# Performance work log

Hardware: AMD Instinct MI355X
Metric: run time of the kernel (lower is better)

Reference implementation:

```python
import jax, jax.numpy as jnp
import numpy as np

B, S, DIM, NH = 256, 64, 1024, 8
DH = DIM // NH
EPS = 1e-6
LN_EPS = 1e-5


def _make_hops(n):
    hops = np.zeros((n, n), dtype=np.int64)
    cur = 1
    for i in range(n):
        for j in range(i + 1, n):
            hops[i, j] = cur
            hops[j, i] = cur
            cur += 1
    return hops, cur


def setup_inputs() -> dict:
    key = jax.random.key(0)
    ks = jax.random.split(key, 8)
    hops_np, curnum = _make_hops(S)
    return {
        "q": jax.random.normal(ks[0], (B, S, DIM), dtype=jnp.float32),
        "k": jax.random.normal(ks[1], (B, S, DIM), dtype=jnp.float32),
        "v": jax.random.normal(ks[2], (B, S, DIM), dtype=jnp.float32),
        "igate_w": jax.random.normal(ks[3], (NH, 3 * DIM), dtype=jnp.float32) * 0.02,
        "igate_b": jax.random.normal(ks[4], (NH,), dtype=jnp.float32) * 0.1,
        "fgate_w": jax.random.normal(ks[5], (NH, 3 * DIM), dtype=jnp.float32) * 0.02,
        "fgate_b": jnp.linspace(3.0, 6.0, NH, dtype=jnp.float32),
        "rpe": jax.random.normal(ks[6], (curnum, DIM), dtype=jnp.float32) * 0.02,
        "ln_w": jax.random.normal(ks[7], (DIM,), dtype=jnp.float32) * 0.1,
        "ln_b": jnp.zeros((DIM,), dtype=jnp.float32),
        "hops": jnp.asarray(hops_np),
    }


def _mlstm_forward(q, k, v, igate_w, igate_b, fgate_w, fgate_b, rpe, ln_w, ln_b, hops):
    Bq, Sq, _ = q.shape
    pos_emb = rpe[hops]                                   # (S, S, DIM)
    gate_in = jnp.concatenate([q, k, v], axis=-1)         # (B, S, 3*DIM)
    ig = gate_in @ igate_w.T + igate_b                    # (B, S, NH)
    fg = gate_in @ fgate_w.T + fgate_b                    # (B, S, NH)
    ig = jnp.transpose(ig, (0, 2, 1))                     # (B, NH, S)
    fg = jnp.transpose(fg, (0, 2, 1))                     # (B, NH, S)

    qh = q.reshape(Bq, Sq, NH, DH).transpose(0, 2, 1, 3)  # (B, NH, S, DH)
    kh = k.reshape(Bq, Sq, NH, DH).transpose(0, 2, 1, 3)
    vh = v.reshape(Bq, Sq, NH, DH).transpose(0, 2, 1, 3)

    # log forget gates, cumulative sum with a leading zero
    log_f = jax.nn.log_sigmoid(fg)                        # (B, NH, S)
    csum = jnp.cumsum(log_f, axis=-1)
    csum = jnp.concatenate([jnp.zeros((Bq, NH, 1), csum.dtype), csum], axis=-1)  # (B,NH,S+1)
    lfm = csum[:, :, :, None] - csum[:, :, None, :]       # (B, NH, S+1, S+1)
    ltr = jnp.tril(jnp.ones((Sq, Sq), dtype=bool))
    log_fg_matrix = jnp.where(ltr, lfm[:, :, 1:, 1:], -jnp.inf)  # (B, NH, S, S)

    log_D = log_fg_matrix + ig[:, :, None, :]             # add i-gate per column
    max_log_D = jnp.max(log_D, axis=-1, keepdims=True)    # rowwise stabilization
    D = jnp.exp(log_D - max_log_D)                        # (B, NH, S, S)

    k_scaled = kh / np.sqrt(DH).astype(np.float32)
    pe = pos_emb.reshape(Sq, Sq, NH, DH)
    k_hop = jnp.einsum('bhvc,vmhc->bhvm', qh, pe)         # (B, NH, S, S)
    qk = jnp.einsum('bhsd,bhtd->bhst', qh, k_scaled)      # (B, NH, S, S)
    C = (qk + k_hop) * D

    normalizer = jnp.maximum(jnp.abs(jnp.sum(C, axis=-1, keepdims=True)), jnp.exp(-max_log_D))
    Cn = C / (normalizer + EPS)
    h = Cn @ vh                                           # (B, NH, S, DH)

    # MultiHeadLayerNorm == group_norm with NH groups: normalize each head over DH
    mu = jnp.mean(h, axis=-1, keepdims=True)
    var = jnp.mean(jnp.square(h - mu), axis=-1, keepdims=True)
    hn = (h - mu) / jnp.sqrt(var + LN_EPS)
    w = (1.0 + ln_w).reshape(NH, DH)                      # residual weight: 1 + w
    b = ln_b.reshape(NH, DH)
    hn = hn * w[None, :, None, :] + b[None, :, None, :]
    return hn.transpose(0, 2, 1, 3).reshape(Bq, Sq, DIM)


def reference(q, k, v, igate_w, igate_b, fgate_w, fgate_b, rpe, ln_w, ln_b, hops):
    return _mlstm_forward(q, k, v, igate_w, igate_b, fgate_w, fgate_b, rpe, ln_w, ln_b, hops)
```

## Files before the change

kernel.cpp:

```cpp
#include <hip/hip_runtime.h>
#include <math.h>

#define BB 256
#define SS 64
#define DIMM 1024
#define NHH 8
#define DHH 128

typedef short bf16x8 __attribute__((ext_vector_type(8)));
typedef float f32x4 __attribute__((ext_vector_type(4)));

__device__ __forceinline__ unsigned cvtpk(float lo, float hi) {
    unsigned r;
    asm("v_cvt_pk_bf16_f32 %0, %1, %2" : "=v"(r) : "v"(lo), "v"(hi));
    return r;
}
__device__ __forceinline__ unsigned pk2(float lo, float hi) { return cvtpk(lo, hi); }
__device__ __forceinline__ unsigned short f2bh(float x) {
    return (unsigned short)(cvtpk(x, 0.0f) & 0xFFFFu);
}
__device__ __forceinline__ float bf2f(unsigned short b) {
    union { unsigned u; float f; } x{((unsigned)b) << 16};
    return x.f;
}
__device__ __forceinline__ void split2(float a, float b, unsigned& hi, unsigned& lo) {
    hi = cvtpk(a, b);
    const float ha = __uint_as_float(hi << 16);
    const float hb = __uint_as_float(hi & 0xFFFF0000u);
    lo = cvtpk(a - ha, b - hb);
}
__device__ __forceinline__ float logsigf(float x) {
    return fminf(x, 0.0f) - log1pf(__expf(-fabsf(x)));
}

__global__ __launch_bounds__(256) void k_gate_mfma(
    const float* __restrict__ q, const float* __restrict__ k, const float* __restrict__ v,
    const float* __restrict__ igw, const float* __restrict__ fgw,
    float* __restrict__ part)
{
    __shared__ unsigned short Xs[64 * 264];
    __shared__ unsigned short Ws[16 * 264];
    const int b = blockIdx.x & 255;
    const int ksl = blockIdx.x >> 8;
    const int t = threadIdx.x;
    const int w = t >> 6, l = t & 63, c = l & 15, g = l >> 4;

    f32x4 acc;
    acc[0] = 0.f; acc[1] = 0.f; acc[2] = 0.f; acc[3] = 0.f;

    for (int step = 0; step < 3; ++step) {
        const int kc = ksl * 3 + step;
        const int tensor = kc >> 2;
        const float* src = (tensor == 0) ? q : (tensor == 1) ? k : v;
        src += ((size_t)b * 64) * 1024 + (kc & 3) * 256;
        {
            const int row = t >> 2, seg = t & 3;
            const float* rp = src + row * 1024;
            #pragma unroll
            for (int e = 0; e < 16; ++e) {
                const int col = e * 16 + seg * 4;
                const float4 x = *reinterpret_cast<const float4*>(rp + col);
                unsigned* dp = reinterpret_cast<unsigned*>(&Xs[row * 264 + col]);
                dp[0] = pk2(x.x, x.y); dp[1] = pk2(x.z, x.w);
            }
        }
        {
            const int o = t >> 4, wseg = t & 15;
            const int p0 = ksl * 768 + step * 256;
            const float* wp = (o < 8 ? igw + o * 3072 : fgw + (o - 8) * 3072) + p0;
            #pragma unroll
            for (int e = 0; e < 4; ++e) {
                const int col = e * 64 + wseg * 4;
                const float4 x = *reinterpret_cast<const float4*>(wp + col);
                unsigned* dp = reinterpret_cast<unsigned*>(&Ws[o * 264 + col]);
                dp[0] = pk2(x.x, x.y); dp[1] = pk2(x.z, x.w);
            }
        }
        __syncthreads();
        #pragma unroll
        for (int kk = 0; kk < 8; ++kk) {
            bf16x8 a  = *reinterpret_cast<const bf16x8*>(&Xs[(16 * w + c) * 264 + 32 * kk + 8 * g]);
            bf16x8 bw = *reinterpret_cast<const bf16x8*>(&Ws[c * 264 + 32 * kk + 8 * g]);
            acc = __builtin_amdgcn_mfma_f32_16x16x32_bf16(a, bw, acc, 0, 0, 0);
        }
        __syncthreads();
    }
    float* pb = part + (((size_t)ksl * 256 + b) * 64) * 16;
    #pragma unroll
    for (int reg = 0; reg < 4; ++reg) {
        const int s = 16 * w + 4 * g + reg;
        pb[s * 16 + c] = acc[reg];
    }
}

__global__ __launch_bounds__(256) void k_gates_final(
    const float* __restrict__ part, const float* __restrict__ igb, const float* __restrict__ fgb,
    float* __restrict__ ig_ws, float* __restrict__ csum_ws, float* __restrict__ pmax_ws)
{
    const int b = blockIdx.x;
    const int t = threadIdx.x;
    __shared__ float red[64][18];
    {
        const int s = t >> 2, oq = t & 3;
        float4 sum = make_float4(0.f, 0.f, 0.f, 0.f);
        #pragma unroll
        for (int ksl = 0; ksl < 4; ++ksl) {
            const float4 p = *reinterpret_cast<const float4*>(
                part + (((size_t)ksl * 256 + b) * 64 + s) * 16 + oq * 4);
            sum.x += p.x; sum.y += p.y; sum.z += p.z; sum.w += p.w;
        }
        red[s][oq * 4 + 0] = sum.x; red[s][oq * 4 + 1] = sum.y;
        red[s][oq * 4 + 2] = sum.z; red[s][oq * 4 + 3] = sum.w;
    }
    __syncthreads();
    if (t < 64) {
        const int s = t;
        #pragma unroll
        for (int h = 0; h < 8; ++h) {
            float ig = red[s][h]     + igb[h];
            float fg = red[s][8 + h] + fgb[h];
            float lf = logsigf(fg);
            float cs = lf;
            #pragma unroll
            for (int d = 1; d < 64; d <<= 1) {
                float o = __shfl_up(cs, (unsigned)d, 64);
                if (s >= d) cs += o;
            }
            float pm = ig - cs;
            #pragma unroll
            for (int d = 1; d < 64; d <<= 1) {
                float o = __shfl_up(pm, (unsigned)d, 64);
                if (s >= d) pm = fmaxf(pm, o);
            }
            const int base = b * NHH + h;
            ig_ws[base * SS + s] = ig;
            csum_ws[base * 65 + s + 1] = cs;
            if (s == 0) csum_ws[base * 65] = 0.0f;
            pmax_ws[base * SS + s] = pm;
        }
    }
}

__global__ __launch_bounds__(256) void k_khop(
    const float* __restrict__ q, const float* __restrict__ rpe, const int* __restrict__ hops,
    float* __restrict__ khop_ws)
{
    __shared__ unsigned short Phi[64 * 136];
    __shared__ unsigned short Plo[64 * 136];
    const int v = blockIdx.x;
    const int h = blockIdx.y;
    const int t = threadIdx.x;
    const int w = t >> 6, l = t & 63, c = l & 15, g = l >> 4;

    const int npair = (v + 1) * 64;
    unsigned* PhiU = reinterpret_cast<unsigned*>(Phi);
    unsigned* PloU = reinterpret_cast<unsigned*>(Plo);
    for (int idx = t; idx < npair; idx += 256) {
        const int m = idx >> 6, cp = idx & 63;
        const float2 x = *reinterpret_cast<const float2*>(
            rpe + (size_t)hops[v * SS + m] * DIMM + h * DHH + 2 * cp);
        unsigned hi, lo;
        split2(x.x, x.y, hi, lo);
        PhiU[m * 68 + cp] = hi;
        PloU[m * 68 + cp] = lo;
    }
    __syncthreads();

    const int ntiles = (v >> 4) + 1;
    union bfu { unsigned u[4]; bf16x8 vv; };
    #pragma unroll
    for (int ms = 0; ms < 4; ++ms) {
        const int brow = 64 * w + 16 * ms + c;
        const float* qbase = q + ((size_t)brow * SS + v) * DIMM + h * DHH + 8 * g;
        bfu qhi[4], qlo[4];
        #pragma unroll
        for (int kk = 0; kk < 4; ++kk) {
            const float4 f0 = *reinterpret_cast<const float4*>(qbase + 32 * kk);
            const float4 f1 = *reinterpret_cast<const float4*>(qbase + 32 * kk + 4);
            split2(f0.x, f0.y, qhi[kk].u[0], qlo[kk].u[0]);
            split2(f0.z, f0.w, qhi[kk].u[1], qlo[kk].u[1]);
            split2(f1.x, f1.y, qhi[kk].u[2], qlo[kk].u[2]);
            split2(f1.z, f1.w, qhi[kk].u[3], qlo[kk].u[3]);
        }
        for (int n = 0; n < ntiles; ++n) {
            f32x4 acc;
            acc[0] = 0.f; acc[1] = 0.f; acc[2] = 0.f; acc[3] = 0.f;
            #pragma unroll
            for (int kk = 0; kk < 4; ++kk) {
                const int off = (16 * n + c) * 136 + 32 * kk + 8 * g;
                bf16x8 bhi = *reinterpret_cast<const bf16x8*>(&Phi[off]);
                bf16x8 blo = *reinterpret_cast<const bf16x8*>(&Plo[off]);
                acc = __builtin_amdgcn_mfma_f32_16x16x32_bf16(qhi[kk].vv, bhi, acc, 0, 0, 0);
                acc = __builtin_amdgcn_mfma_f32_16x16x32_bf16(qlo[kk].vv, bhi, acc, 0, 0, 0);
                acc = __builtin_amdgcn_mfma_f32_16x16x32_bf16(qhi[kk].vv, blo, acc, 0, 0, 0);
            }
            #pragma unroll
            for (int reg = 0; reg < 4; ++reg) {
                const int bo = 64 * w + 16 * ms + 4 * g + reg;
                khop_ws[(((size_t)bo * NHH + h) * SS + v) * SS + 16 * n + c] = acc[reg];
            }
        }
    }
}

__global__ __launch_bounds__(256) void k_attn(
    const float* __restrict__ q, const float* __restrict__ k, const float* __restrict__ v,
    const float* __restrict__ lnw, const float* __restrict__ lnb,
    const float* __restrict__ ig_ws, const float* __restrict__ csum_ws,
    const float* __restrict__ pmax_ws, const float* __restrict__ khop_ws,
    float* __restrict__ out)
{
    __shared__ __attribute__((aligned(16))) unsigned short Kspl[2 * 64 * 136];
    __shared__ float csum_s[65];
    __shared__ float ig_s[64];
    __shared__ float pmax_s[64];
    __shared__ float lnw_s[128];
    __shared__ float lnb_s[128];

    const int bid = blockIdx.x;
    const int b = bid >> 3, h = bid & 7;
    const int t = threadIdx.x;
    const int w = t >> 6, l = t & 63, c = l & 15, g = l >> 4;
    const float rs_dh = 0.08838834764831845f;

    unsigned short* Khi = Kspl;
    unsigned short* Klo = Kspl + 64 * 136;

    float4 vreg[2][4];
    #pragma unroll
    for (int it = 0; it < 2; ++it) {
        const int u = t + 256 * it;
        const int jp = u >> 4, seg8 = u & 15;
        const float* r0 = v + ((size_t)(b * 64 + 2 * jp)) * 1024 + h * 128 + seg8 * 8;
        vreg[it][0] = *reinterpret_cast<const float4*>(r0);
        vreg[it][1] = *reinterpret_cast<const float4*>(r0 + 4);
        vreg[it][2] = *reinterpret_cast<const float4*>(r0 + 1024);
        vreg[it][3] = *reinterpret_cast<const float4*>(r0 + 1028);
    }

    float kh[4][4];
    {
        const float* khb = khop_ws + ((size_t)(b * NHH + h) * SS) * SS;
        #pragma unroll
        for (int n = 0; n < 4; ++n) {
            if (n > w) continue;
            #pragma unroll
            for (int reg = 0; reg < 4; ++reg) {
                const int i = 16 * w + 4 * g + reg;
                kh[n][reg] = khb[(size_t)i * SS + 16 * n + c];
            }
        }
    }

    #pragma unroll
    for (int it = 0; it < 2; ++it) {
        const int u = t + 256 * it;
        const int row = u >> 3, seg = u & 7;
        const float* kp = k + ((size_t)(b * 64 + row)) * 1024 + h * 128;
        #pragma unroll
        for (int e = 0; e < 2; ++e) {
            const int col = e * 64 + seg * 8;
            const float4 ya = *reinterpret_cast<const float4*>(kp + col);
            const float4 yb = *reinterpret_cast<const float4*>(kp + col + 4);
            unsigned* dh = reinterpret_cast<unsigned*>(&Khi[row * 136 + col]);
            unsigned* dl = reinterpret_cast<unsigned*>(&Klo[row * 136 + col]);
            split2(ya.x * rs_dh, ya.y * rs_dh, dh[0], dl[0]);
            split2(ya.z * rs_dh, ya.w * rs_dh, dh[1], dl[1]);
            split2(yb.x * rs_dh, yb.y * rs_dh, dh[2], dl[2]);
            split2(yb.z * rs_dh, yb.w * rs_dh, dh[3], dl[3]);
        }
    }
    const int cb = b * NHH + h;
    if (t < 65) csum_s[t] = csum_ws[cb * 65 + t];
    if (t >= 128 && t < 192) ig_s[t - 128] = ig_ws[cb * SS + (t - 128)];
    if (t >= 192) pmax_s[t - 192] = pmax_ws[cb * SS + (t - 192)];
    if (t < 128) lnw_s[t] = lnw[h * 128 + t];
    else if (t < 256) lnb_s[t - 128] = lnb[h * 128 + (t - 128)];

    union bfu { unsigned u[4]; bf16x8 v; };
    bfu qhi[4], qlo[4];
    {
        const int qrow = 16 * w + c;
        const float* qbase = q + ((size_t)(b * 64 + qrow)) * 1024 + h * 128 + 8 * g;
        #pragma unroll
        for (int kk = 0; kk < 4; ++kk) {
            const float4 f0 = *reinterpret_cast<const float4*>(qbase + 32 * kk);
            const float4 f1 = *reinterpret_cast<const float4*>(qbase + 32 * kk + 4);
            split2(f0.x, f0.y, qhi[kk].u[0], qlo[kk].u[0]);
            split2(f0.z, f0.w, qhi[kk].u[1], qlo[kk].u[1]);
            split2(f1.x, f1.y, qhi[kk].u[2], qlo[kk].u[2]);
            split2(f1.z, f1.w, qhi[kk].u[3], qlo[kk].u[3]);
        }
    }
    __syncthreads();

    f32x4 acc[4];
    #pragma unroll
    for (int n = 0; n < 4; ++n) { acc[n][0]=0.f; acc[n][1]=0.f; acc[n][2]=0.f; acc[n][3]=0.f; }
    #pragma unroll
    for (int kk = 0; kk < 4; ++kk) {
        #pragma unroll
        for (int n = 0; n < 4; ++n) {
            if (n > w) continue;
            const int off = (16 * n + c) * 136 + 32 * kk + 8 * g;
            bf16x8 bhi = *reinterpret_cast<const bf16x8*>(&Khi[off]);
            bf16x8 blo = *reinterpret_cast<const bf16x8*>(&Klo[off]);
            acc[n] = __builtin_amdgcn_mfma_f32_16x16x32_bf16(qhi[kk].v, bhi, acc[n], 0, 0, 0);
            acc[n] = __builtin_amdgcn_mfma_f32_16x16x32_bf16(qlo[kk].v, bhi, acc[n], 0, 0, 0);
            acc[n] = __builtin_amdgcn_mfma_f32_16x16x32_bf16(qhi[kk].v, blo, acc[n], 0, 0, 0);
        }
    }
    __syncthreads();

    unsigned short* VT = Kspl;
    unsigned short* Cn = Kspl + 128 * 72;
    #pragma unroll
    for (int it = 0; it < 2; ++it) {
        const int u = t + 256 * it;
        const int jp = u >> 4, seg8 = u & 15;
        float v0[8], v1[8];
        v0[0]=vreg[it][0].x; v0[1]=vreg[it][0].y; v0[2]=vreg[it][0].z; v0[3]=vreg[it][0].w;
        v0[4]=vreg[it][1].x; v0[5]=vreg[it][1].y; v0[6]=vreg[it][1].z; v0[7]=vreg[it][1].w;
        v1[0]=vreg[it][2].x; v1[1]=vreg[it][2].y; v1[2]=vreg[it][2].z; v1[3]=vreg[it][2].w;
        v1[4]=vreg[it][3].x; v1[5]=vreg[it][3].y; v1[6]=vreg[it][3].z; v1[7]=vreg[it][3].w;
        #pragma unroll
        for (int m = 0; m < 8; ++m) {
            const int cc = seg8 * 8 + m;
            unsigned byte = (unsigned)(cc * 144 + 4 * jp);
            byte ^= ((cc >> 3) & 7) << 4;
            *reinterpret_cast<unsigned*>(reinterpret_cast<char*>(VT) + byte) = pk2(v0[m], v1[m]);
        }
    }

    {
        float mi[4], rs[4];
        #pragma unroll
        for (int reg = 0; reg < 4; ++reg) {
            const int i = 16 * w + 4 * g + reg;
            mi[reg] = csum_s[i + 1] + pmax_s[i];
            rs[reg] = 0.0f;
        }
        #pragma unroll
        for (int n = 0; n < 4; ++n) {
            if (n > w) continue;
            const int j = 16 * n + c;
            const float cj = csum_s[j + 1], igj = ig_s[j];
            #pragma unroll
            for (int reg = 0; reg < 4; ++reg) {
                const int i = 16 * w + 4 * g + reg;
                float val = 0.0f;
                if (j <= i) {
                    const float sc = acc[n][reg] + kh[n][reg];
                    val = sc * __expf(csum_s[i + 1] - cj + igj - mi[reg]);
                }
                acc[n][reg] = val;
                rs[reg] += val;
            }
        }
        #pragma unroll
        for (int reg = 0; reg < 4; ++reg) {
            float r = rs[reg];
            r += __shfl_xor(r, 1); r += __shfl_xor(r, 2);
            r += __shfl_xor(r, 4); r += __shfl_xor(r, 8);
            const float nrm = fmaxf(fabsf(r), __expf(-mi[reg]));
            const float inv = 1.0f / (nrm + 1e-6f);
            const int i = 16 * w + 4 * g + reg;
            #pragma unroll
            for (int n = 0; n < 4; ++n) {
                const int j = 16 * n + c;
                Cn[i * 72 + j] = f2bh(acc[n][reg] * inv);
            }
        }
    }
    __syncthreads();

    f32x4 hacc[8];
    #pragma unroll
    for (int n = 0; n < 8; ++n) { hacc[n][0]=0.f; hacc[n][1]=0.f; hacc[n][2]=0.f; hacc[n][3]=0.f; }
    #pragma unroll
    for (int ks = 0; ks < 2; ++ks) {
        bf16x8 a = *reinterpret_cast<const bf16x8*>(&Cn[(16 * w + c) * 72 + 32 * ks + 8 * g]);
        #pragma unroll
        for (int n = 0; n < 8; ++n) {
            const int cc = 16 * n + c;
            unsigned byte = (unsigned)(cc * 144 + 64 * ks + 16 * g);
            byte ^= ((cc >> 3) & 7) << 4;
            bf16x8 bv = *reinterpret_cast<const bf16x8*>(reinterpret_cast<const char*>(VT) + byte);
            hacc[n] = __builtin_amdgcn_mfma_f32_16x16x32_bf16(a, bv, hacc[n], 0, 0, 0);
        }
    }

    #pragma unroll
    for (int reg = 0; reg < 4; ++reg) {
        float s1 = 0.f, s2 = 0.f;
        #pragma unroll
        for (int n = 0; n < 8; ++n) { const float x = hacc[n][reg]; s1 += x; s2 = fmaf(x, x, s2); }
        s1 += __shfl_xor(s1, 1); s1 += __shfl_xor(s1, 2);
        s1 += __shfl_xor(s1, 4); s1 += __shfl_xor(s1, 8);
        s2 += __shfl_xor(s2, 1); s2 += __shfl_xor(s2, 2);
        s2 += __shfl_xor(s2, 4); s2 += __shfl_xor(s2, 8);
        const float mu = s1 * (1.0f / 128.0f);
        const float var = s2 * (1.0f / 128.0f) - mu * mu;
        const float rstd = rsqrtf(var + 1e-5f);
        const int io = 16 * w + 4 * g + reg;
        float* op = out + (((size_t)(b * 64 + io)) * 8 + h) * 128;
        #pragma unroll
        for (int n = 0; n < 8; ++n) {
            const int cc = 16 * n + c;
            op[cc] = (hacc[n][reg] - mu) * rstd * (1.0f + lnw_s[cc]) + lnb_s[cc];
        }
    }
}

extern "C" void kernel_launch(void* const* d_in, const int* in_sizes, int n_in,
                              void* d_out, int out_size, void* d_ws, size_t ws_size,
                              hipStream_t stream) {
    const float* q   = (const float*)d_in[0];
    const float* k   = (const float*)d_in[1];
    const float* v   = (const float*)d_in[2];
    const float* igw = (const float*)d_in[3];
    const float* igb = (const float*)d_in[4];
    const float* fgw = (const float*)d_in[5];
    const float* fgb = (const float*)d_in[6];
    const float* rpe = (const float*)d_in[7];
    const float* lnw = (const float*)d_in[8];
    const float* lnb = (const float*)d_in[9];
    const int*  hops = (const int*)d_in[10];
    float* out = (float*)d_out;

    float* ig_ws   = (float*)d_ws;
    float* pmax_ws = ig_ws + 131072;
    float* csum_ws = pmax_ws + 131072;
    float* part    = csum_ws + 133120;
    float* khop_ws = part;

    hipLaunchKernelGGL(k_gate_mfma, dim3(1024), dim3(256), 0, stream,
                       q, k, v, igw, fgw, part);
    hipLaunchKernelGGL(k_gates_final, dim3(BB), dim3(256), 0, stream,
                       part, igb, fgb, ig_ws, csum_ws, pmax_ws);
    hipLaunchKernelGGL(k_khop, dim3(SS, NHH), dim3(256), 0, stream,
                       q, rpe, hops, khop_ws);
    hipLaunchKernelGGL(k_attn, dim3(BB * NHH), dim3(256), 0, stream,
                       q, k, v, lnw, lnb, ig_ws, csum_ws, pmax_ws, khop_ws, out);
}
```

Baseline: 129.9 us.

## Load gate GEMM operands directly into MFMA registers and double K-split

The gate projection kernel now has each lane load its fp32 operand fragments straight from global memory, convert them to bf16 in registers and feed the MFMA. This removes the LDS staging buffers and the block barriers. The K dimension is split into 8 slices instead of 4, so 2048 blocks launch and the reduction kernel sums 8 partials. Each lane now reads 32-byte strided chunks rather than coalesced rows, and the partial buffer doubles in size, which could collide with workspace reused for khop.

```diff
diff --git a/kernel.cpp b/kernel.cpp
--- a/kernel.cpp
+++ b/kernel.cpp
@@ -38,52 +38,33 @@
     const float* __restrict__ igw, const float* __restrict__ fgw,
     float* __restrict__ part)
 {
-    __shared__ unsigned short Xs[64 * 264];
-    __shared__ unsigned short Ws[16 * 264];
     const int b = blockIdx.x & 255;
     const int ksl = blockIdx.x >> 8;
     const int t = threadIdx.x;
     const int w = t >> 6, l = t & 63, c = l & 15, g = l >> 4;
 
+    const size_t arow = (size_t)(b * 64 + 16 * w + c) * 1024;
+    const float* wrow = (c < 8) ? (igw + c * 3072) : (fgw + (c - 8) * 3072);
+
     f32x4 acc;
     acc[0] = 0.f; acc[1] = 0.f; acc[2] = 0.f; acc[3] = 0.f;
 
-    for (int step = 0; step < 3; ++step) {
-        const int kc = ksl * 3 + step;
-        const int tensor = kc >> 2;
+    union bfu { unsigned u[4]; bf16x8 v; };
+    #pragma unroll 4
+    for (int kk = 0; kk < 12; ++kk) {
+        const int p = ksl * 384 + 32 * kk + 8 * g;
+        const int tensor = p >> 10, col = p & 1023;
         const float* src = (tensor == 0) ? q : (tensor == 1) ? k : v;
-        src += ((size_t)b * 64) * 1024 + (kc & 3) * 256;
-        {
-            const int row = t >> 2, seg = t & 3;
-            const float* rp = src + row * 1024;
-            #pragma unroll
-            for (int e = 0; e < 16; ++e) {
-                const int col = e * 16 + seg * 4;
-                const float4 x = *reinterpret_cast<const float4*>(rp + col);
-                unsigned* dp = reinterpret_cast<unsigned*>(&Xs[row * 264 + col]);
-                dp[0] = pk2(x.x, x.y); dp[1] = pk2(x.z, x.w);
-            }
-        }
-        {
-            const int o = t >> 4, wseg = t & 15;
-            const int p0 = ksl * 768 + step * 256;
-            const float* wp = (o < 8 ? igw + o * 3072 : fgw + (o - 8) * 3072) + p0;
-            #pragma unroll
-            for (int e = 0; e < 4; ++e) {
-                const int col = e * 64 + wseg * 4;
-                const float4 x = *reinterpret_cast<const float4*>(wp + col);
-                unsigned* dp = reinterpret_cast<unsigned*>(&Ws[o * 264 + col]);
-                dp[0] = pk2(x.x, x.y); dp[1] = pk2(x.z, x.w);
-            }
-        }
-        __syncthreads();
-        #pragma unroll
-        for (int kk = 0; kk < 8; ++kk) {
-            bf16x8 a  = *reinterpret_cast<const bf16x8*>(&Xs[(16 * w + c) * 264 + 32 * kk + 8 * g]);
-            bf16x8 bw = *reinterpret_cast<const bf16x8*>(&Ws[c * 264 + 32 * kk + 8 * g]);
-            acc = __builtin_amdgcn_mfma_f32_16x16x32_bf16(a, bw, acc, 0, 0, 0);
-        }
-        __syncthreads();
+        const float4 a0 = *reinterpret_cast<const float4*>(src + arow + col);
+        const float4 a1 = *reinterpret_cast<const float4*>(src + arow + col + 4);
+        const float4 b0 = *reinterpret_cast<const float4*>(wrow + p);
+        const float4 b1 = *reinterpret_cast<const float4*>(wrow + p + 4);
+        bfu af, bf;
+        af.u[0] = pk2(a0.x, a0.y); af.u[1] = pk2(a0.z, a0.w);
+        af.u[2] = pk2(a1.x, a1.y); af.u[3] = pk2(a1.z, a1.w);
+        bf.u[0] = pk2(b0.x, b0.y); bf.u[1] = pk2(b0.z, b0.w);
+        bf.u[2] = pk2(b1.x, b1.y); bf.u[3] = pk2(b1.z, b1.w);
+        acc = __builtin_amdgcn_mfma_f32_16x16x32_bf16(af.v, bf.v, acc, 0, 0, 0);
     }
     float* pb = part + (((size_t)ksl * 256 + b) * 64) * 16;
     #pragma unroll
@@ -104,7 +85,7 @@
         const int s = t >> 2, oq = t & 3;
         float4 sum = make_float4(0.f, 0.f, 0.f, 0.f);
         #pragma unroll
-        for (int ksl = 0; ksl < 4; ++ksl) {
+        for (int ksl = 0; ksl < 8; ++ksl) {
             const float4 p = *reinterpret_cast<const float4*>(
                 part + (((size_t)ksl * 256 + b) * 64 + s) * 16 + oq * 4);
             sum.x += p.x; sum.y += p.y; sum.z += p.z; sum.w += p.w;
@@ -434,7 +415,7 @@
     float* part    = csum_ws + 133120;
     float* khop_ws = part;
 
-    hipLaunchKernelGGL(k_gate_mfma, dim3(1024), dim3(256), 0, stream,
+    hipLaunchKernelGGL(k_gate_mfma, dim3(2048), dim3(256), 0, stream,
                        q, k, v, igw, fgw, part);
     hipLaunchKernelGGL(k_gates_final, dim3(BB), dim3(256), 0, stream,
                        part, igb, fgb, ig_ws, csum_ws, pmax_ws);
```

New measurement: 144.5 us. 11.2% more time.
